# Kernel optimization log

Hardware: AMD Instinct MI355X
Metric: run time of the kernel (lower is better)

## Reference

```python
import jax, jax.numpy as jnp
import numpy as np


def setup_inputs() -> dict:
    key = jax.random.key(0)
    k1, k2 = jax.random.split(key)
    x = jax.random.normal(k1, (8, 64, 256, 256), dtype=jnp.float32)
    grid = jax.random.normal(k2, (8, 256, 256, 2), dtype=jnp.float32)
    return {"x": x, "grid": grid}


def _warp_bilinear_zeros(x, grid):
    # x: [N, C, H, W]; grid: [N, Ho, Wo, 2] with (dx, dy) pixel offsets.
    N, C, H, W = x.shape
    Ho, Wo = grid.shape[1], grid.shape[2]
    dt = grid.dtype
    base_y = jnp.arange(Ho, dtype=dt)[:, None]   # [Ho, 1]
    base_x = jnp.arange(Wo, dtype=dt)[None, :]   # [1, Wo]
    abs_x = grid[..., 0] + base_x                # [N, Ho, Wo]
    abs_y = grid[..., 1] + base_y
    # normalize then unnormalize (align_corners=True), matching the torch chain
    norm_x = abs_x * 2 / (W - 1) - 1
    norm_y = abs_y * 2 / (H - 1) - 1
    ix = (norm_x + 1) * 0.5 * (W - 1)
    iy = (norm_y + 1) * 0.5 * (H - 1)

    x0 = jnp.floor(ix); x1 = x0 + 1
    y0 = jnp.floor(iy); y1 = y0 + 1
    wx1 = ix - x0; wx0 = 1 - wx1
    wy1 = iy - y0; wy0 = 1 - wy1

    inb_x0 = (x0 >= 0) & (x0 <= W - 1)
    inb_x1 = (x1 >= 0) & (x1 <= W - 1)
    inb_y0 = (y0 >= 0) & (y0 <= H - 1)
    inb_y1 = (y1 >= 0) & (y1 <= H - 1)

    xi0 = jnp.clip(x0, 0, W - 1).astype(jnp.int32)
    xi1 = jnp.clip(x1, 0, W - 1).astype(jnp.int32)
    yi0 = jnp.clip(y0, 0, H - 1).astype(jnp.int32)
    yi1 = jnp.clip(y1, 0, H - 1).astype(jnp.int32)

    def gather(img, yi, xi):  # img [C,H,W], yi/xi [Ho,Wo] -> [C,Ho,Wo]
        return img[:, yi, xi]
    g = jax.vmap(gather)

    # zeros padding: mask out-of-bounds corner contributions
    w00 = (wy0 * wx0 * (inb_y0 & inb_x0).astype(dt))[:, None]  # [N,1,Ho,Wo]
    w01 = (wy0 * wx1 * (inb_y0 & inb_x1).astype(dt))[:, None]
    w10 = (wy1 * wx0 * (inb_y1 & inb_x0).astype(dt))[:, None]
    w11 = (wy1 * wx1 * (inb_y1 & inb_x1).astype(dt))[:, None]

    out = (g(x, yi0, xi0) * w00 + g(x, yi0, xi1) * w01
           + g(x, yi1, xi0) * w10 + g(x, yi1, xi1) * w11)
    return out  # [N, C, Ho, Wo]


def reference(x, grid):
    return _warp_bilinear_zeros(x, grid)
```

## Files before the change

kernel.cpp:

```cpp
#include <hip/hip_runtime.h>


#define N_ 8
#define C_ 64
#define H_ 256
#define W_ 256
#define HO_ 256
#define WO_ 256
#define CCH 8
#define NCC (C_ / CCH)

typedef float f2v __attribute__((ext_vector_type(2)));

__global__ __launch_bounds__(256) void gridsample_kernel(
    const float* __restrict__ x,
    const float2* __restrict__ grid2,
    float* __restrict__ out)
{
    const int b    = blockIdx.x;
    const int xcd  = b & 7;
    const int idx  = b >> 3;
    const int plane = xcd * (NCC * N_ / 8) + (idx >> 8);
    const int ho   = idx & 255;
    const int n    = plane >> 3;
    const int cc   = plane & 7;
    const int wo   = threadIdx.x;

    const int sp = (n * HO_ + ho) * WO_ + wo;
    const float2 g = grid2[sp];

    const float absx = g.x + (float)wo;
    const float absy = g.y + (float)ho;
    const float normx = absx * 2.0f / (float)(W_ - 1) - 1.0f;
    const float normy = absy * 2.0f / (float)(H_ - 1) - 1.0f;
    const float ix = (normx + 1.0f) * 0.5f * (float)(W_ - 1);
    const float iy = (normy + 1.0f) * 0.5f * (float)(H_ - 1);

    const float x0f = floorf(ix);
    const float y0f = floorf(iy);
    const float x1f = x0f + 1.0f;
    const float y1f = y0f + 1.0f;

    const float wx1 = ix - x0f, wx0 = 1.0f - wx1;
    const float wy1 = iy - y0f, wy0 = 1.0f - wy1;

    const float hx0 = ((x0f >= 0.0f) && (x0f <= (float)(W_ - 1))) ? wx0 : 0.0f;
    const float hx1 = ((x1f >= 0.0f) && (x1f <= (float)(W_ - 1))) ? wx1 : 0.0f;
    const float ey0 = ((y0f >= 0.0f) && (y0f <= (float)(H_ - 1))) ? wy0 : 0.0f;
    const float ey1 = ((y1f >= 0.0f) && (y1f <= (float)(H_ - 1))) ? wy1 : 0.0f;

    const int xlo = (int)fminf(fmaxf(x0f, 0.0f), (float)(W_ - 2));
    const bool hi = (x0f >= (float)(W_ - 1));
    const bool lo = (x0f <= -1.0f);
    const float A = (hi ? 0.0f : hx0) + (lo ? hx1 : 0.0f);
    const float B = (hi ? hx0 : 0.0f) + (lo ? 0.0f : hx1);

    const float W00 = A * ey0, W01 = B * ey0;
    const float W10 = A * ey1, W11 = B * ey1;

    const int yr0 = min(max((int)y0f, 0), H_ - 1);
    const int yr1 = min(max((int)y1f, 0), H_ - 1);
    const int r0 = yr0 * W_ + xlo;
    const int r1 = yr1 * W_ + xlo;

    const int c0 = cc * CCH;
    const float* __restrict__ xb =
        x + ((size_t)n * C_ + c0) * (H_ * W_);
    float* __restrict__ ob =
        out + (((size_t)n * C_ + c0) * HO_ + ho) * WO_ + wo;

    #pragma unroll
    for (int c = 0; c < CCH; ++c) {
        const float* __restrict__ xc = xb + (size_t)c * (H_ * W_);
        f2v v0, v1;
        __builtin_memcpy(&v0, xc + r0, 8);
        __builtin_memcpy(&v1, xc + r1, 8);
        const float val = v0.x * W00 + v0.y * W01
                        + v1.x * W10 + v1.y * W11;
        ob[(size_t)c * (HO_ * WO_)] = val;
    }
}

extern "C" void kernel_launch(void* const* d_in, const int* in_sizes, int n_in,
                              void* d_out, int out_size, void* d_ws, size_t ws_size,
                              hipStream_t stream) {
    const float*  x    = (const float*)d_in[0];
    const float2* grid = (const float2*)d_in[1];
    float*        out  = (float*)d_out;

    const int nblocks = N_ * NCC * HO_;
    gridsample_kernel<<<nblocks, 256, 0, stream>>>(x, grid, out);
}
```

Before: 282.8 us.

## Stage per-block input row window in LDS with double-buffered async loads

Each block first reduces the minimum and maximum source rows its 256 outputs touch. It then copies that row window (up to 12 rows) per channel into LDS using global_load_lds, double-buffered across the 8 channels, and does the bilinear taps from LDS. Samples that fall outside the window take a global-load fallback path. The goal is to replace scattered per-lane global gathers with coalesced full-row loads. The cost is loading whole rows (more bytes than the old gather) plus extra block-wide barriers per channel.

New measurement: 291.8 us. 1.03x slower.

```diff
diff --git a/kernel.cpp b/kernel.cpp
--- a/kernel.cpp
+++ b/kernel.cpp
@@ -9,22 +9,27 @@
 #define WO_ 256
 #define CCH 8
 #define NCC (C_ / CCH)
-
-typedef float f2v __attribute__((ext_vector_type(2)));
+#define RMAX 12
+#define LDSW 260
 
 __global__ __launch_bounds__(256) void gridsample_kernel(
     const float* __restrict__ x,
     const float2* __restrict__ grid2,
     float* __restrict__ out)
 {
-    const int b    = blockIdx.x;
-    const int xcd  = b & 7;
-    const int idx  = b >> 3;
+    __shared__ __attribute__((aligned(16))) float sm[2][RMAX * LDSW];
+    __shared__ int swin[8];
+
+    const int b     = blockIdx.x;
+    const int xcd   = b & 7;
+    const int idx   = b >> 3;
     const int plane = xcd * (NCC * N_ / 8) + (idx >> 8);
-    const int ho   = idx & 255;
-    const int n    = plane >> 3;
-    const int cc   = plane & 7;
-    const int wo   = threadIdx.x;
+    const int ho    = idx & 255;
+    const int n     = plane >> 3;
+    const int cc    = plane & 7;
+    const int wo    = threadIdx.x;
+    const int ln    = threadIdx.x & 63;
+    const int wv    = threadIdx.x >> 6;
 
     const int sp = (n * HO_ + ho) * WO_ + wo;
     const float2 g = grid2[sp];
@@ -60,6 +65,24 @@
 
     const int yr0 = min(max((int)y0f, 0), H_ - 1);
     const int yr1 = min(max((int)y1f, 0), H_ - 1);
+
+    int lmin = yr0, lmax = yr1;
+    #pragma unroll
+    for (int m = 32; m >= 1; m >>= 1) {
+        lmin = min(lmin, __shfl_xor(lmin, m));
+        lmax = max(lmax, __shfl_xor(lmax, m));
+    }
+    if (ln == 0) { swin[wv] = lmin; swin[4 + wv] = lmax; }
+    __syncthreads();
+    const int wlo  = min(min(swin[0], swin[1]), min(swin[2], swin[3]));
+    const int whi0 = max(max(swin[4], swin[5]), max(swin[6], swin[7]));
+    const int whi  = min(whi0, wlo + RMAX - 1);
+    const int R    = whi - wlo + 1;
+
+    const int o0 = min(yr0 - wlo, RMAX - 1) * LDSW + xlo;
+    const int o1 = min(yr1 - wlo, RMAX - 1) * LDSW + xlo;
+    const bool oow0 = yr0 > whi;
+    const bool oow1 = yr1 > whi;
     const int r0 = yr0 * W_ + xlo;
     const int r1 = yr1 * W_ + xlo;
 
@@ -69,15 +92,49 @@
     float* __restrict__ ob =
         out + (((size_t)n * C_ + c0) * HO_ + ho) * WO_ + wo;
 
+    for (int r = wv; r < R; r += 4) {
+        const float* gp = xb + (size_t)(wlo + r) * W_ + ln * 4;
+        __builtin_amdgcn_global_load_lds(
+            (const __attribute__((address_space(1))) void*)gp,
+            (__attribute__((address_space(3))) void*)&sm[0][r * LDSW],
+            16, 0, 0);
+    }
+    __syncthreads();
+
     #pragma unroll
     for (int c = 0; c < CCH; ++c) {
-        const float* __restrict__ xc = xb + (size_t)c * (H_ * W_);
-        f2v v0, v1;
-        __builtin_memcpy(&v0, xc + r0, 8);
-        __builtin_memcpy(&v1, xc + r1, 8);
-        const float val = v0.x * W00 + v0.y * W01
-                        + v1.x * W10 + v1.y * W11;
-        ob[(size_t)c * (HO_ * WO_)] = val;
+        if (c + 1 < CCH) {
+            const float* xn = xb + (size_t)(c + 1) * (H_ * W_);
+            for (int r = wv; r < R; r += 4) {
+                const float* gp = xn + (size_t)(wlo + r) * W_ + ln * 4;
+                __builtin_amdgcn_global_load_lds(
+                    (const __attribute__((address_space(1))) void*)gp,
+                    (__attribute__((address_space(3))) void*)&sm[(c + 1) & 1][r * LDSW],
+                    16, 0, 0);
+            }
+        }
+
+        const float* smb = sm[c & 1];
+        float p00 = smb[o0];
+        float p01 = smb[o0 + 1];
+        float p10 = smb[o1];
+        float p11 = smb[o1 + 1];
+
+        if (__builtin_expect(oow0, 0)) {
+            const float* xc = xb + (size_t)c * (H_ * W_);
+            p00 = xc[r0];
+            p01 = xc[r0 + 1];
+        }
+        if (__builtin_expect(oow1, 0)) {
+            const float* xc = xb + (size_t)c * (H_ * W_);
+            p10 = xc[r1];
+            p11 = xc[r1 + 1];
+        }
+
+        ob[(size_t)c * (HO_ * WO_)] =
+            p00 * W00 + p01 * W01 + p10 * W10 + p11 * W11;
+
+        if (c + 1 < CCH) __syncthreads();
     }
 }
 
```
